# Kernel optimization log

Measured on AMD Instinct MI355X. Metric: run time of the kernel, lower is better.

## Reference

```python
import jax, jax.numpy as jnp
import numpy as np

HEADS = 4
DIM_HEAD = 32
SCALE = DIM_HEAD ** -0.5


def setup_inputs() -> dict:
    key = jax.random.key(0)
    k1, k2, k3 = jax.random.split(key, 3)
    dim, hidden = 256, HEADS * DIM_HEAD
    x = jax.random.normal(k1, (4, dim, 64, 64), dtype=jnp.float32)
    w_qkv = jax.random.normal(k2, (hidden * 3, dim), dtype=jnp.float32) * (dim ** -0.5)
    w_out = jax.random.normal(k3, (dim, hidden), dtype=jnp.float32) * (hidden ** -0.5)
    b_out = jnp.zeros((dim,), dtype=jnp.float32)
    return {"x": x, "w_qkv": w_qkv, "w_out": w_out, "b_out": b_out}


def reference(x, w_qkv, w_out, b_out):
    b, c, h, w = x.shape
    # 1x1 conv (no bias) == channel matmul
    qkv = jnp.einsum('bchw,oc->bohw', x, w_qkv)           # [b, 3*hidden, h, w]
    q, k, v = jnp.split(qkv, 3, axis=1)
    def to_heads(t):
        # [b, heads*d, h, w] -> [b, heads, h*w, d]
        return t.reshape(b, HEADS, DIM_HEAD, h * w).transpose(0, 1, 3, 2)
    q, k, v = to_heads(q) * SCALE, to_heads(k), to_heads(v)
    sim = jnp.einsum('bhid,bhjd->bhij', q, k)             # [b, heads, hw, hw]
    attn = jax.nn.softmax(sim, axis=-1)
    out = jnp.einsum('bhij,bhjd->bhid', attn, v)          # [b, heads, hw, d]
    out = out.transpose(0, 1, 3, 2).reshape(b, HEADS * DIM_HEAD, h, w)
    # output 1x1 conv with bias
    return jnp.einsum('bchw,oc->bohw', out, w_out) + b_out[None, :, None, None]
```

## Files before the change

### kernel.cpp

```cpp
#include <hip/hip_runtime.h>
#include <hip/hip_fp16.h>

#define HEADS 4
#define DH    32
#define HW    4096
#define CIN   256
#define HID   128

using half8   = __attribute__((ext_vector_type(8))) _Float16;
using half4   = __attribute__((ext_vector_type(4))) _Float16;
using floatx4 = __attribute__((ext_vector_type(4))) float;

#define SHIFT2 4.328085122666891f

__global__ __launch_bounds__(256) void conv_x(
    const float* __restrict__ x, _Float16* __restrict__ Xh)
{
  __shared__ float t[64][65];
  const int b = blockIdx.z, ct = blockIdx.y, pt = blockIdx.x;
  const int tid = threadIdx.x;
  const float* src = x + ((size_t)(b * CIN + ct * 64)) * HW + pt * 64;
  #pragma unroll
  for (int i = 0; i < 16; ++i) {
    int idx = tid + i * 256;
    int c = idx >> 6, p = idx & 63;
    t[c][p] = src[(size_t)c * HW + p];
  }
  __syncthreads();
  #pragma unroll
  for (int pass = 0; pass < 2; ++pass) {
    int p = (tid >> 3) + pass * 32;
    int c0 = (tid & 7) * 8;
    half8 v;
    #pragma unroll
    for (int j = 0; j < 8; ++j) v[j] = (_Float16)t[c0 + j][p];
    *(half8*)(Xh + ((size_t)(b * HW + pt * 64 + p)) * CIN + ct * 64 + c0) = v;
  }
}

__global__ __launch_bounds__(256) void conv_w(
    const float* __restrict__ wq, const float* __restrict__ wo,
    _Float16* __restrict__ Wh, _Float16* __restrict__ Woh)
{
  const int idx = blockIdx.x * 256 + threadIdx.x;
  const int n1 = 384 * CIN;
  if (idx < n1) {
    float s = (idx < 128 * CIN) ? 0.25508275947f : 1.0f;
    Wh[idx] = (_Float16)(wq[idx] * s);
  } else {
    Woh[idx - n1] = (_Float16)wo[idx - n1];
  }
}

__global__ __launch_bounds__(256) void qkv_gemm(
    const _Float16* __restrict__ Wh, const _Float16* __restrict__ Xh,
    _Float16* __restrict__ Qw, _Float16* __restrict__ Kw,
    _Float16* __restrict__ Vtw)
{
  __shared__ _Float16 As[64][136];
  __shared__ _Float16 Bs[64][136];
  const int mt = blockIdx.x, nt = blockIdx.y;
  const int b = nt >> 6, p0 = (nt & 63) * 64;
  const int tid = threadIdx.x;
  const int wv = tid >> 6, lane = tid & 63, lm = lane & 15, quad = lane >> 4;

  const _Float16* A = Wh + (size_t)mt * 64 * CIN;
  const _Float16* B = Xh + ((size_t)b * HW + p0) * CIN;

  floatx4 acc[4] = {{0,0,0,0},{0,0,0,0},{0,0,0,0},{0,0,0,0}};

  #pragma unroll
  for (int kh = 0; kh < 2; ++kh) {
    __syncthreads();
    #pragma unroll
    for (int i = 0; i < 4; ++i) {
      int ci = tid + i * 256;
      int r = ci >> 4, c8 = (ci & 15) * 8;
      *(half8*)&As[r][c8] = *(const half8*)(A + (size_t)r * CIN + kh * 128 + c8);
      *(half8*)&Bs[r][c8] = *(const half8*)(B + (size_t)r * CIN + kh * 128 + c8);
    }
    __syncthreads();
    #pragma unroll
    for (int ks = 0; ks < 4; ++ks) {
      half8 a = *(const half8*)&As[wv * 16 + lm][ks * 32 + quad * 8];
      #pragma unroll
      for (int ns = 0; ns < 4; ++ns) {
        half8 bf = *(const half8*)&Bs[ns * 16 + lm][ks * 32 + quad * 8];
        acc[ns] = __builtin_amdgcn_mfma_f32_16x16x32_f16(a, bf, acc[ns], 0, 0, 0);
      }
    }
  }

  const int sec = mt >> 1;
  const int o_base = (mt & 1) * 64 + wv * 16 + quad * 4;
  const int hh = o_base >> 5, dd = o_base & 31;
  const int bh = b * HEADS + hh;
  if (sec < 2) {
    _Float16* dst = (sec == 0) ? Qw : Kw;
    #pragma unroll
    for (int ns = 0; ns < 4; ++ns) {
      int p = p0 + ns * 16 + lm;
      half4 v = {(_Float16)acc[ns][0], (_Float16)acc[ns][1],
                 (_Float16)acc[ns][2], (_Float16)acc[ns][3]};
      *(half4*)(dst + ((size_t)bh * HW + p) * DH + dd) = v;
    }
  } else {
    #pragma unroll
    for (int ns = 0; ns < 4; ++ns) {
      int p = p0 + ns * 16 + lm;
      #pragma unroll
      for (int r = 0; r < 4; ++r)
        Vtw[((size_t)bh * DH + dd + r) * HW + p] = (_Float16)acc[ns][r];
    }
  }
}

__global__ __launch_bounds__(256) void attn(
    const _Float16* __restrict__ Qw, const _Float16* __restrict__ Kw,
    const _Float16* __restrict__ Vtw, _Float16* __restrict__ Ot)
{
  __shared__ _Float16 ks[2][64][40];
  __shared__ _Float16 vt[2][32][72];

  const int bh = blockIdx.y, qt = blockIdx.x;
  const int tid = threadIdx.x;
  const int wv = tid >> 6, lane = tid & 63, lm = lane & 15, quad = lane >> 4;

  const _Float16* qptr = Qw + ((size_t)bh * HW + qt * 64 + wv * 16 + lm) * DH + quad * 8;
  const half8 qa = *(const half8*)qptr;

  const _Float16 one = (_Float16)1.0f;
  const half4 ones4 = {one, one, one, one};

  floatx4 oT[2] = {{0,0,0,0},{0,0,0,0}};
  floatx4 l4    = {0,0,0,0};

  const _Float16* kbase = Kw  + (size_t)bh * HW * DH;
  const _Float16* vbase = Vtw + (size_t)bh * DH * HW;
  const int kr = tid >> 2, kc = (tid & 3) * 8;
  const int vr = tid >> 3, vc = (tid & 7) * 8;

  half8 kpre = *(const half8*)(kbase + (size_t)kr * DH + kc);
  half8 vpre = *(const half8*)(vbase + (size_t)vr * HW + vc);
  *(half8*)&ks[0][kr][kc] = kpre;
  *(half8*)&vt[0][vr][vc] = vpre;
  kpre = *(const half8*)(kbase + ((size_t)64 + kr) * DH + kc);
  vpre = *(const half8*)(vbase + (size_t)vr * HW + 64 + vc);
  __syncthreads();

  for (int kt = 0; kt < HW / 64; ++kt) {
    const int cur = kt & 1;
    *(half8*)&ks[cur ^ 1][kr][kc] = kpre;
    *(half8*)&vt[cur ^ 1][vr][vc] = vpre;
    kpre = *(const half8*)(kbase + ((size_t)(kt + 2) * 64 + kr) * DH + kc);
    vpre = *(const half8*)(vbase + (size_t)vr * HW + (kt + 2) * 64 + vc);

    floatx4 sT[4];
    #pragma unroll
    for (int f = 0; f < 4; ++f) {
      half8 kb = *(const half8*)&ks[cur][f * 16 + lm][quad * 8];
      floatx4 z = {0,0,0,0};
      sT[f] = __builtin_amdgcn_mfma_f32_16x16x32_f16(kb, qa, z, 0, 0, 0);
    }

    #pragma unroll
    for (int f = 0; f < 4; ++f) {
      half4 pb;
      #pragma unroll
      for (int r = 0; r < 4; ++r)
        pb[r] = (_Float16)__builtin_amdgcn_exp2f(sT[f][r] - SHIFT2);
      l4 = __builtin_amdgcn_mfma_f32_16x16x16f16(ones4, pb, l4, 0, 0, 0);
      #pragma unroll
      for (int g = 0; g < 2; ++g) {
        half4 va = *(const half4*)&vt[cur][g * 16 + lm][f * 16 + quad * 4];
        oT[g] = __builtin_amdgcn_mfma_f32_16x16x16f16(va, pb, oT[g], 0, 0, 0);
      }
    }
    __syncthreads();
  }

  const float inv = 1.0f / l4[0];
  const int b = bh >> 2, hh = bh & 3;
  _Float16* obase = Ot + ((size_t)(b * HW + qt * 64 + wv * 16 + lm)) * HID + hh * DH;
  #pragma unroll
  for (int g = 0; g < 2; ++g) {
    half4 v = {(_Float16)(oT[g][0] * inv), (_Float16)(oT[g][1] * inv),
               (_Float16)(oT[g][2] * inv), (_Float16)(oT[g][3] * inv)};
    *(half4*)(obase + g * 16 + quad * 4) = v;
  }
}

__global__ __launch_bounds__(256) void out_gemm(
    const _Float16* __restrict__ Woh, const _Float16* __restrict__ Ot,
    const float* __restrict__ bo, float* __restrict__ out)
{
  __shared__ _Float16 As[64][136];
  __shared__ _Float16 Bs[64][136];
  __shared__ float os[64][68];
  const int mt = blockIdx.x, nt = blockIdx.y;
  const int b = nt >> 6, p0 = (nt & 63) * 64;
  const int tid = threadIdx.x;
  const int wv = tid >> 6, lane = tid & 63, lm = lane & 15, quad = lane >> 4;

  const _Float16* A = Woh + (size_t)mt * 64 * HID;
  const _Float16* B = Ot + ((size_t)b * HW + p0) * HID;

  #pragma unroll
  for (int i = 0; i < 4; ++i) {
    int ci = tid + i * 256;
    int r = ci >> 4, c8 = (ci & 15) * 8;
    *(half8*)&As[r][c8] = *(const half8*)(A + (size_t)r * HID + c8);
    *(half8*)&Bs[r][c8] = *(const half8*)(B + (size_t)r * HID + c8);
  }
  __syncthreads();

  floatx4 acc[4] = {{0,0,0,0},{0,0,0,0},{0,0,0,0},{0,0,0,0}};
  #pragma unroll
  for (int ks = 0; ks < 4; ++ks) {
    half8 a = *(const half8*)&As[wv * 16 + lm][ks * 32 + quad * 8];
    #pragma unroll
    for (int ns = 0; ns < 4; ++ns) {
      half8 bf = *(const half8*)&Bs[ns * 16 + lm][ks * 32 + quad * 8];
      acc[ns] = __builtin_amdgcn_mfma_f32_16x16x32_f16(a, bf, acc[ns], 0, 0, 0);
    }
  }

  #pragma unroll
  for (int ns = 0; ns < 4; ++ns)
    #pragma unroll
    for (int r = 0; r < 4; ++r)
      os[wv * 16 + quad * 4 + r][ns * 16 + lm] = acc[ns][r];
  __syncthreads();

  const int o = tid >> 2, pq = (tid & 3) * 16;
  const float bias = bo[mt * 64 + o];
  float* dst = out + ((size_t)(b * CIN + mt * 64 + o)) * HW + p0 + pq;
  #pragma unroll
  for (int j = 0; j < 4; ++j) {
    float4 v = *(const float4*)&os[o][pq + j * 4];
    v.x += bias; v.y += bias; v.z += bias; v.w += bias;
    *(float4*)(dst + j * 4) = v;
  }
}

extern "C" void kernel_launch(void* const* d_in, const int* in_sizes, int n_in,
                              void* d_out, int out_size, void* d_ws, size_t ws_size,
                              hipStream_t stream)
{
  const float* x     = (const float*)d_in[0];
  const float* w_qkv = (const float*)d_in[1];
  const float* w_out = (const float*)d_in[2];
  const float* b_out = (const float*)d_in[3];
  float* out = (float*)d_out;

  char* ws = (char*)d_ws;
  _Float16* Xh  = (_Float16*)(ws);
  _Float16* Ot  = (_Float16*)(ws);
  _Float16* Qw  = (_Float16*)(ws + (8u  << 20));
  _Float16* Kw  = (_Float16*)(ws + (12u << 20));
  _Float16* Vtw = (_Float16*)(ws + (16u << 20));
  _Float16* Wh  = (_Float16*)(ws + (20u << 20));
  _Float16* Woh = (_Float16*)(ws + (20u << 20) + (256u << 10));

  dim3 blk(256);
  conv_x<<<dim3(64, 4, 4), blk, 0, stream>>>(x, Xh);
  conv_w<<<dim3(512), blk, 0, stream>>>(w_qkv, w_out, Wh, Woh);
  qkv_gemm<<<dim3(6, 256), blk, 0, stream>>>(Wh, Xh, Qw, Kw, Vtw);
  attn<<<dim3(64, 16), blk, 0, stream>>>(Qw, Kw, Vtw, Ot);
  out_gemm<<<dim3(4, 256), blk, 0, stream>>>(Woh, Ot, b_out, out);
}
```

Before: 167.6 us.

## Fuse input/weight fp16 conversion into GEMMs and double attention K/V tile per sync

Drops the separate conv_x and conv_w kernels. The QKV GEMM now reads fp32 x and weights directly, transposing and converting through shared memory in 64-channel chunks, and the output GEMM converts its fp32 weights inline. The attention kernel now processes two 64-key subtiles per barrier with deeper register prefetch, and folds the softmax shift into the MFMA accumulator initializer. This removes two launches and the intermediate fp16 round trips, at the cost of redundant x conversion across the 6 M-tiles, more barriers in the QKV GEMM, and doubled attention LDS use.

Measured after the change: 165.4 us. No clear change (-1.3%).

```diff
diff --git a/kernel.cpp b/kernel.cpp
--- a/kernel.cpp
+++ b/kernel.cpp
@@ -12,76 +12,62 @@
 using floatx4 = __attribute__((ext_vector_type(4))) float;
 
 #define SHIFT2 4.328085122666891f
-
-__global__ __launch_bounds__(256) void conv_x(
-    const float* __restrict__ x, _Float16* __restrict__ Xh)
-{
-  __shared__ float t[64][65];
-  const int b = blockIdx.z, ct = blockIdx.y, pt = blockIdx.x;
-  const int tid = threadIdx.x;
-  const float* src = x + ((size_t)(b * CIN + ct * 64)) * HW + pt * 64;
-  #pragma unroll
-  for (int i = 0; i < 16; ++i) {
-    int idx = tid + i * 256;
-    int c = idx >> 6, p = idx & 63;
-    t[c][p] = src[(size_t)c * HW + p];
-  }
-  __syncthreads();
-  #pragma unroll
-  for (int pass = 0; pass < 2; ++pass) {
-    int p = (tid >> 3) + pass * 32;
-    int c0 = (tid & 7) * 8;
-    half8 v;
-    #pragma unroll
-    for (int j = 0; j < 8; ++j) v[j] = (_Float16)t[c0 + j][p];
-    *(half8*)(Xh + ((size_t)(b * HW + pt * 64 + p)) * CIN + ct * 64 + c0) = v;
-  }
-}
-
-__global__ __launch_bounds__(256) void conv_w(
-    const float* __restrict__ wq, const float* __restrict__ wo,
-    _Float16* __restrict__ Wh, _Float16* __restrict__ Woh)
-{
-  const int idx = blockIdx.x * 256 + threadIdx.x;
-  const int n1 = 384 * CIN;
-  if (idx < n1) {
-    float s = (idx < 128 * CIN) ? 0.25508275947f : 1.0f;
-    Wh[idx] = (_Float16)(wq[idx] * s);
-  } else {
-    Woh[idx - n1] = (_Float16)wo[idx - n1];
-  }
-}
-
-__global__ __launch_bounds__(256) void qkv_gemm(
-    const _Float16* __restrict__ Wh, const _Float16* __restrict__ Xh,
+#define WQSCALE 0.25508275947f
+
+__global__ __launch_bounds__(256) void qkv_fused(
+    const float* __restrict__ w, const float* __restrict__ x,
     _Float16* __restrict__ Qw, _Float16* __restrict__ Kw,
     _Float16* __restrict__ Vtw)
 {
-  __shared__ _Float16 As[64][136];
-  __shared__ _Float16 Bs[64][136];
+  __shared__ float t[64][65];
+  __shared__ _Float16 As[64][72];
+  __shared__ _Float16 Bs[64][72];
   const int mt = blockIdx.x, nt = blockIdx.y;
   const int b = nt >> 6, p0 = (nt & 63) * 64;
   const int tid = threadIdx.x;
   const int wv = tid >> 6, lane = tid & 63, lm = lane & 15, quad = lane >> 4;
-
-  const _Float16* A = Wh + (size_t)mt * 64 * CIN;
-  const _Float16* B = Xh + ((size_t)b * HW + p0) * CIN;
+  const float wscale = (mt < 2) ? WQSCALE : 1.0f;
+
+  const float* Ag = w + (size_t)(mt * 64) * CIN;
+  const float* xb = x + (size_t)b * CIN * HW + p0;
 
   floatx4 acc[4] = {{0,0,0,0},{0,0,0,0},{0,0,0,0},{0,0,0,0}};
 
-  #pragma unroll
-  for (int kh = 0; kh < 2; ++kh) {
+  for (int kq = 0; kq < 4; ++kq) {
     __syncthreads();
     #pragma unroll
     for (int i = 0; i < 4; ++i) {
       int ci = tid + i * 256;
-      int r = ci >> 4, c8 = (ci & 15) * 8;
-      *(half8*)&As[r][c8] = *(const half8*)(A + (size_t)r * CIN + kh * 128 + c8);
-      *(half8*)&Bs[r][c8] = *(const half8*)(B + (size_t)r * CIN + kh * 128 + c8);
-    }
-    __syncthreads();
-    #pragma unroll
-    for (int ks = 0; ks < 4; ++ks) {
+      int cc = ci >> 4, p4 = (ci & 15) * 4;
+      *(float4*)&t[cc][p4] =
+          *(const float4*)(xb + (size_t)(kq * 64 + cc) * HW + p4);
+    }
+    #pragma unroll
+    for (int i = 0; i < 2; ++i) {
+      int ci = tid + i * 256;
+      int r = ci >> 3, c8 = (ci & 7) * 8;
+      const float* src = Ag + (size_t)r * CIN + kq * 64 + c8;
+      float4 u0 = *(const float4*)(src);
+      float4 u1 = *(const float4*)(src + 4);
+      half8 h = {(_Float16)(u0.x * wscale), (_Float16)(u0.y * wscale),
+                 (_Float16)(u0.z * wscale), (_Float16)(u0.w * wscale),
+                 (_Float16)(u1.x * wscale), (_Float16)(u1.y * wscale),
+                 (_Float16)(u1.z * wscale), (_Float16)(u1.w * wscale)};
+      *(half8*)&As[r][c8] = h;
+    }
+    __syncthreads();
+    #pragma unroll
+    for (int i = 0; i < 2; ++i) {
+      int idx = tid + i * 256;
+      int p = idx >> 3, c0 = (idx & 7) * 8;
+      half8 v;
+      #pragma unroll
+      for (int k = 0; k < 8; ++k) v[k] = (_Float16)t[c0 + k][p];
+      *(half8*)&Bs[p][c0] = v;
+    }
+    __syncthreads();
+    #pragma unroll
+    for (int ks = 0; ks < 2; ++ks) {
       half8 a = *(const half8*)&As[wv * 16 + lm][ks * 32 + quad * 8];
       #pragma unroll
       for (int ns = 0; ns < 4; ++ns) {
@@ -119,8 +105,8 @@
     const _Float16* __restrict__ Qw, const _Float16* __restrict__ Kw,
     const _Float16* __restrict__ Vtw, _Float16* __restrict__ Ot)
 {
-  __shared__ _Float16 ks[2][64][40];
-  __shared__ _Float16 vt[2][32][72];
+  __shared__ _Float16 ks[2][2][64][40];
+  __shared__ _Float16 vt[2][2][32][72];
 
   const int bh = blockIdx.y, qt = blockIdx.x;
   const int tid = threadIdx.x;
@@ -131,6 +117,7 @@
 
   const _Float16 one = (_Float16)1.0f;
   const half4 ones4 = {one, one, one, one};
+  const floatx4 shiftc = {-SHIFT2, -SHIFT2, -SHIFT2, -SHIFT2};
 
   floatx4 oT[2] = {{0,0,0,0},{0,0,0,0}};
   floatx4 l4    = {0,0,0,0};
@@ -140,40 +127,52 @@
   const int kr = tid >> 2, kc = (tid & 3) * 8;
   const int vr = tid >> 3, vc = (tid & 7) * 8;
 
-  half8 kpre = *(const half8*)(kbase + (size_t)kr * DH + kc);
-  half8 vpre = *(const half8*)(vbase + (size_t)vr * HW + vc);
-  *(half8*)&ks[0][kr][kc] = kpre;
-  *(half8*)&vt[0][vr][vc] = vpre;
-  kpre = *(const half8*)(kbase + ((size_t)64 + kr) * DH + kc);
-  vpre = *(const half8*)(vbase + (size_t)vr * HW + 64 + vc);
+  half8 kA = *(const half8*)(kbase + (size_t)kr * DH + kc);
+  half8 vA = *(const half8*)(vbase + (size_t)vr * HW + vc);
+  half8 kB = *(const half8*)(kbase + ((size_t)64 + kr) * DH + kc);
+  half8 vB = *(const half8*)(vbase + (size_t)vr * HW + 64 + vc);
+  *(half8*)&ks[0][0][kr][kc] = kA;
+  *(half8*)&vt[0][0][vr][vc] = vA;
+  *(half8*)&ks[0][1][kr][kc] = kB;
+  *(half8*)&vt[0][1][vr][vc] = vB;
+  kA = *(const half8*)(kbase + ((size_t)128 + kr) * DH + kc);
+  vA = *(const half8*)(vbase + (size_t)vr * HW + 128 + vc);
+  kB = *(const half8*)(kbase + ((size_t)192 + kr) * DH + kc);
+  vB = *(const half8*)(vbase + (size_t)vr * HW + 192 + vc);
   __syncthreads();
 
-  for (int kt = 0; kt < HW / 64; ++kt) {
-    const int cur = kt & 1;
-    *(half8*)&ks[cur ^ 1][kr][kc] = kpre;
-    *(half8*)&vt[cur ^ 1][vr][vc] = vpre;
-    kpre = *(const half8*)(kbase + ((size_t)(kt + 2) * 64 + kr) * DH + kc);
-    vpre = *(const half8*)(vbase + (size_t)vr * HW + (kt + 2) * 64 + vc);
-
-    floatx4 sT[4];
-    #pragma unroll
-    for (int f = 0; f < 4; ++f) {
-      half8 kb = *(const half8*)&ks[cur][f * 16 + lm][quad * 8];
-      floatx4 z = {0,0,0,0};
-      sT[f] = __builtin_amdgcn_mfma_f32_16x16x32_f16(kb, qa, z, 0, 0, 0);
-    }
-
-    #pragma unroll
-    for (int f = 0; f < 4; ++f) {
-      half4 pb;
-      #pragma unroll
-      for (int r = 0; r < 4; ++r)
-        pb[r] = (_Float16)__builtin_amdgcn_exp2f(sT[f][r] - SHIFT2);
-      l4 = __builtin_amdgcn_mfma_f32_16x16x16f16(ones4, pb, l4, 0, 0, 0);
-      #pragma unroll
-      for (int g = 0; g < 2; ++g) {
-        half4 va = *(const half4*)&vt[cur][g * 16 + lm][f * 16 + quad * 4];
-        oT[g] = __builtin_amdgcn_mfma_f32_16x16x16f16(va, pb, oT[g], 0, 0, 0);
+  for (int it = 0; it < HW / 128; ++it) {
+    const int ph = it & 1, nx = ph ^ 1;
+    *(half8*)&ks[nx][0][kr][kc] = kA;
+    *(half8*)&vt[nx][0][vr][vc] = vA;
+    *(half8*)&ks[nx][1][kr][kc] = kB;
+    *(half8*)&vt[nx][1][vr][vc] = vB;
+    const size_t koff = (size_t)(it * 2 + 4) * 64;
+    kA = *(const half8*)(kbase + (koff + kr) * DH + kc);
+    vA = *(const half8*)(vbase + (size_t)vr * HW + koff + vc);
+    kB = *(const half8*)(kbase + (koff + 64 + kr) * DH + kc);
+    vB = *(const half8*)(vbase + (size_t)vr * HW + koff + 64 + vc);
+
+    #pragma unroll
+    for (int sub = 0; sub < 2; ++sub) {
+      floatx4 sT[4];
+      #pragma unroll
+      for (int f = 0; f < 4; ++f) {
+        half8 kb = *(const half8*)&ks[ph][sub][f * 16 + lm][quad * 8];
+        sT[f] = __builtin_amdgcn_mfma_f32_16x16x32_f16(kb, qa, shiftc, 0, 0, 0);
+      }
+      #pragma unroll
+      for (int f = 0; f < 4; ++f) {
+        half4 pb;
+        #pragma unroll
+        for (int r = 0; r < 4; ++r)
+          pb[r] = (_Float16)__builtin_amdgcn_exp2f(sT[f][r]);
+        l4 = __builtin_amdgcn_mfma_f32_16x16x16f16(ones4, pb, l4, 0, 0, 0);
+        #pragma unroll
+        for (int g = 0; g < 2; ++g) {
+          half4 va = *(const half4*)&vt[ph][sub][g * 16 + lm][f * 16 + quad * 4];
+          oT[g] = __builtin_amdgcn_mfma_f32_16x16x16f16(va, pb, oT[g], 0, 0, 0);
+        }
       }
     }
     __syncthreads();
@@ -191,7 +190,7 @@
 }
 
 __global__ __launch_bounds__(256) void out_gemm(
-    const _Float16* __restrict__ Woh, const _Float16* __restrict__ Ot,
+    const float* __restrict__ wo, const _Float16* __restrict__ Ot,
     const float* __restrict__ bo, float* __restrict__ out)
 {
   __shared__ _Float16 As[64][136];
@@ -202,14 +201,19 @@
   const int tid = threadIdx.x;
   const int wv = tid >> 6, lane = tid & 63, lm = lane & 15, quad = lane >> 4;
 
-  const _Float16* A = Woh + (size_t)mt * 64 * HID;
+  const float* Ag = wo + (size_t)(mt * 64) * HID;
   const _Float16* B = Ot + ((size_t)b * HW + p0) * HID;
 
   #pragma unroll
   for (int i = 0; i < 4; ++i) {
     int ci = tid + i * 256;
     int r = ci >> 4, c8 = (ci & 15) * 8;
-    *(half8*)&As[r][c8] = *(const half8*)(A + (size_t)r * HID + c8);
+    const float* src = Ag + (size_t)r * HID + c8;
+    float4 u0 = *(const float4*)(src);
+    float4 u1 = *(const float4*)(src + 4);
+    half8 h = {(_Float16)u0.x, (_Float16)u0.y, (_Float16)u0.z, (_Float16)u0.w,
+               (_Float16)u1.x, (_Float16)u1.y, (_Float16)u1.z, (_Float16)u1.w};
+    *(half8*)&As[r][c8] = h;
     *(half8*)&Bs[r][c8] = *(const half8*)(B + (size_t)r * HID + c8);
   }
   __syncthreads();
@@ -254,18 +258,13 @@
   float* out = (float*)d_out;
 
   char* ws = (char*)d_ws;
-  _Float16* Xh  = (_Float16*)(ws);
   _Float16* Ot  = (_Float16*)(ws);
   _Float16* Qw  = (_Float16*)(ws + (8u  << 20));
   _Float16* Kw  = (_Float16*)(ws + (12u << 20));
   _Float16* Vtw = (_Float16*)(ws + (16u << 20));
-  _Float16* Wh  = (_Float16*)(ws + (20u << 20));
-  _Float16* Woh = (_Float16*)(ws + (20u << 20) + (256u << 10));
 
   dim3 blk(256);
-  conv_x<<<dim3(64, 4, 4), blk, 0, stream>>>(x, Xh);
-  conv_w<<<dim3(512), blk, 0, stream>>>(w_qkv, w_out, Wh, Woh);
-  qkv_gemm<<<dim3(6, 256), blk, 0, stream>>>(Wh, Xh, Qw, Kw, Vtw);
+  qkv_fused<<<dim3(6, 256), blk, 0, stream>>>(w_qkv, x, Qw, Kw, Vtw);
   attn<<<dim3(64, 16), blk, 0, stream>>>(Qw, Kw, Vtw, Ot);
-  out_gemm<<<dim3(4, 256), blk, 0, stream>>>(Woh, Ot, b_out, out);
-}
+  out_gemm<<<dim3(4, 256), blk, 0, stream>>>(w_out, Ot, b_out, out);
+}
```
